# Performance work log

Measured on AMD Instinct MI355X. Metric: run time of the kernel, lower is better.

The kernel has to match this reference:

```python
import jax, jax.numpy as jnp
import numpy as np

TAU = 0.1
HARD_K = 32
MIN_OVERLAP = 4
PAIR_WEIGHTS = [("view", "cart", 0.2), ("cart", "purchase", 1.0), ("view", "purchase", 1.0)]


def setup_inputs() -> dict:
    key = jax.random.key(0)
    ks = jax.random.split(key, 6)
    U, D = 100000, 128
    return {
        "emb_view": jax.random.normal(ks[0], (U, D), dtype=jnp.float32),
        "emb_cart": jax.random.normal(ks[1], (U, D), dtype=jnp.float32),
        "emb_purchase": jax.random.normal(ks[2], (U, D), dtype=jnp.float32),
        "users_view": jax.random.randint(ks[3], (20000,), 0, U, dtype=jnp.int64),
        "users_cart": jax.random.randint(ks[4], (15000,), 0, U, dtype=jnp.int64),
        "users_purchase": jax.random.randint(ks[5], (10000,), 0, U, dtype=jnp.int64),
    }


def _l2norm(x):
    # F.normalize(x, dim=-1): x / max(||x||, eps)
    n = jnp.linalg.norm(x, axis=-1, keepdims=True)
    return x / jnp.maximum(n, 1e-12)


def _directional(z_weak, z_strong, tau, hard_k):
    N = z_strong.shape[0]
    if N < 2:
        return jnp.zeros((), dtype=z_strong.dtype)
    z_w = _l2norm(jax.lax.stop_gradient(z_weak))  # weak side is detached
    z_s = _l2norm(z_strong)
    sim = (z_s @ z_w.T) / tau  # [N, N]
    pos = jnp.diagonal(sim)    # positive logits, labels = arange(N)
    n_hard = min(hard_k, N - 1)
    if 0 < n_hard < N - 1:
        neg_only = jnp.where(jnp.eye(N, dtype=bool), -jnp.inf, sim)
        hard_neg, _ = jax.lax.top_k(neg_only, n_hard)          # [N, n_hard]
        logits = jnp.concatenate([pos[:, None], hard_neg], 1)  # [N, 1+n_hard]
        return jnp.mean(jax.scipy.special.logsumexp(logits, axis=1) - pos)
    # full-softmax CE with label i for row i
    return jnp.mean(jax.scipy.special.logsumexp(sim, axis=1) - pos)


def reference(emb_view, emb_cart, emb_purchase, users_view, users_cart, users_purchase):
    embs = {"view": emb_view, "cart": emb_cart, "purchase": emb_purchase}
    users = {
        "view": np.asarray(users_view),
        "cart": np.asarray(users_cart),
        "purchase": np.asarray(users_purchase),
    }
    loss = jnp.zeros((), dtype=emb_view.dtype)
    for weak, strong, w in PAIR_WEIGHTS:
        u_w, u_s = users[weak], users[strong]
        if u_w.size == 0 or u_s.size == 0:
            continue
        # common_pair = u_w[isin(u_w, u_s)] : keeps u_w order and duplicates
        common = u_w[np.isin(u_w, u_s)]
        if common.size < MIN_OVERLAP:
            continue
        idx = jnp.asarray(common)
        loss = loss + w * _directional(embs[weak][idx], embs[strong][idx], TAU, HARD_K)
    return loss
```

## Files before the change

kernel.cpp:

```cpp
#include <hip/hip_runtime.h>
#include <hip/hip_bf16.h>
#include <math.h>

#define D 128
#define NEG_INF (-3.0e38f)
#define LDA 136
#define MAGIC 0x5CA1AB1Eu

#define C0 3200
#define C1 1792
#define C2 2304
#define T0 25
#define T1 14
#define T2 18
#define NTILES (T0 * T0 + T1 * T1 + T2 * T2)
#define NSEL (C0 / 4 + C1 / 4 + C2 / 4)

typedef __attribute__((ext_vector_type(8))) short bf16x8;
typedef __attribute__((ext_vector_type(8))) unsigned short u16x8;
typedef __attribute__((ext_vector_type(4))) float f32x4;

__device__ __forceinline__ float wredf_add(float v) {
#pragma unroll
  for (int m = 32; m; m >>= 1) v += __shfl_xor(v, m, 64);
  return v;
}
__device__ __forceinline__ float wredf_max(float v) {
#pragma unroll
  for (int m = 32; m; m >>= 1) v = fmaxf(v, __shfl_xor(v, m, 64));
  return v;
}
__device__ __forceinline__ float wredf_min(float v) {
#pragma unroll
  for (int m = 32; m; m >>= 1) v = fminf(v, __shfl_xor(v, m, 64));
  return v;
}
__device__ __forceinline__ int wredi_add(int v) {
#pragma unroll
  for (int m = 32; m; m >>= 1) v += __shfl_xor(v, m, 64);
  return v;
}
__device__ __forceinline__ double wredd_add(double v) {
#pragma unroll
  for (int m = 32; m; m >>= 1) v += __shfl_xor(v, m, 64);
  return v;
}

__global__ void masks_k(const int* __restrict__ uc, int nc,
                        const int* __restrict__ up, int npu,
                        unsigned* __restrict__ mc, unsigned* __restrict__ mp,
                        unsigned long long* __restrict__ header) {
  if (blockIdx.x == 0) header[threadIdx.x] = 0ull;
  int t = blockIdx.x * blockDim.x + threadIdx.x;
  if (t < nc) {
    mc[uc[t]] = MAGIC;
  } else {
    int t2 = t - nc;
    if (t2 < npu) mp[up[t2]] = MAGIC;
  }
}

struct FGArgs {
  const int* src[3];
  int n[3];
  const unsigned* mask[3];
  const float* embW[3];
  const float* embS[3];
  short* zw[3];
  short* zs[3];
  int cap[3];
  int seg1, seg2;
  int* counts;
};

__global__ __launch_bounds__(256) void filtgather_k(FGArgs a) {
  int t = blockIdx.x * 256 + threadIdx.x;
  int lane = threadIdx.x & 63;
  int s, base;
  if (t < a.seg1) { s = 0; base = t; }
  else if (t < a.seg2) { s = 1; base = t - a.seg1; }
  else { s = 2; base = t - a.seg2; }
  bool match = false;
  int u = 0;
  if (base < a.n[s]) {
    u = a.src[s][base];
    match = (a.mask[s][u] == MAGIC);
  }
  unsigned long long b = __ballot(match);
  int tot = __popcll(b);
  if (!tot) return;
  int idx0 = 0;
  if (lane == 0) idx0 = atomicAdd(a.counts + s, tot);
  idx0 = __shfl(idx0, 0, 64);
  const float* eW = a.embW[s];
  const float* eS = a.embS[s];
  short* zw = a.zw[s];
  short* zs = a.zs[s];
  int cap = a.cap[s];
  unsigned long long bb = b;
  for (int k = 0; k < tot; ++k) {
    int sl = __builtin_ctzll(bb);
    bb &= bb - 1;
    int p = idx0 + k;
    if (p >= cap) break;
    int uu = __shfl(u, sl, 64);
    float2 vw = *(const float2*)(eW + (size_t)uu * D + lane * 2);
    float2 vs = *(const float2*)(eS + (size_t)uu * D + lane * 2);
    float ssw = wredf_add(vw.x * vw.x + vw.y * vw.y);
    float sss = wredf_add(vs.x * vs.x + vs.y * vs.y);
    float iw = 1.0f / fmaxf(sqrtf(ssw), 1e-12f);
    float is = 1.0f / fmaxf(sqrtf(sss), 1e-12f);
    __hip_bfloat16 w0 = __float2bfloat16(vw.x * iw), w1 = __float2bfloat16(vw.y * iw);
    __hip_bfloat16 s0 = __float2bfloat16(vs.x * is), s1 = __float2bfloat16(vs.y * is);
    *(ushort2*)(zw + (size_t)p * D + lane * 2) =
        make_ushort2(*(unsigned short*)&w0, *(unsigned short*)&w1);
    *(ushort2*)(zs + (size_t)p * D + lane * 2) =
        make_ushort2(*(unsigned short*)&s0, *(unsigned short*)&s1);
  }
}

struct GemmArgs {
  const short *zs0, *zw0, *zs1, *zw1, *zs2, *zw2;
  unsigned short *s0, *s1, *s2;
  const int* counts;
};

__device__ __forceinline__ void gemm_tile(const short* __restrict__ A, const short* __restrict__ B,
                                          unsigned short* __restrict__ C, int ldc, int bx, int by,
                                          int N, short* As, short* Bs, int tid) {
  int rb = by * 128, cb = bx * 128;
  if (rb >= N || cb >= N) return;
  int rrow = tid >> 4, rcol = (tid & 15) * 8;
#pragma unroll
  for (int pass = 0; pass < 8; ++pass) {
    int row = pass * 16 + rrow;
    uint4 va = *(const uint4*)(A + (size_t)(rb + row) * D + rcol);
    uint4 vb = *(const uint4*)(B + (size_t)(cb + row) * D + rcol);
    *(uint4*)(&As[row * LDA + rcol]) = va;
    *(uint4*)(&Bs[row * LDA + rcol]) = vb;
  }
  __syncthreads();
  int wave = tid >> 6, lane = tid & 63;
  int wr = (wave >> 1) * 64, wc = (wave & 1) * 64;
  int ln = lane & 15, quad = lane >> 4;
  f32x4 acc[4][4] = {};
#pragma unroll
  for (int ks = 0; ks < 4; ++ks) {
    int ko = ks * 32 + quad * 8;
    bf16x8 af[4], bg[4];
#pragma unroll
    for (int i = 0; i < 4; ++i) af[i] = *(const bf16x8*)(&As[(wr + i * 16 + ln) * LDA + ko]);
#pragma unroll
    for (int j = 0; j < 4; ++j) bg[j] = *(const bf16x8*)(&Bs[(wc + j * 16 + ln) * LDA + ko]);
#pragma unroll
    for (int i = 0; i < 4; ++i)
#pragma unroll
      for (int j = 0; j < 4; ++j)
        acc[i][j] = __builtin_amdgcn_mfma_f32_16x16x32_bf16(af[i], bg[j], acc[i][j], 0, 0, 0);
  }
  __syncthreads();
#pragma unroll
  for (int i = 0; i < 4; ++i)
#pragma unroll
    for (int j = 0; j < 4; ++j) {
      int tcol = wc + j * 16 + ln;
#pragma unroll
      for (int r = 0; r < 4; ++r) {
        int trow = wr + i * 16 + quad * 4 + r;
        __hip_bfloat16 h = __float2bfloat16(acc[i][j][r] * 10.0f);
        As[trow * LDA + tcol] = *(short*)&h;
      }
    }
  __syncthreads();
#pragma unroll
  for (int pass = 0; pass < 8; ++pass) {
    int idx = pass * 256 + tid;
    int row = idx >> 4, c8 = (idx & 15) * 8;
    *(uint4*)(C + (size_t)(rb + row) * ldc + cb + c8) = *(const uint4*)(&As[row * LDA + c8]);
  }
  __syncthreads();
}

__global__ __launch_bounds__(256) void gemm_all_k(GemmArgs g) {
  __shared__ __align__(16) short As[128 * LDA];
  __shared__ __align__(16) short Bs[128 * LDA];
  int tid = threadIdx.x;
  int b = blockIdx.x;
  if (b < T0 * T0) {
    int N = min(g.counts[0], C0);
    gemm_tile(g.zs0, g.zw0, g.s0, C0, b % T0, b / T0, N, As, Bs, tid);
  } else if (b < T0 * T0 + T1 * T1) {
    int t = b - T0 * T0;
    int N = min(g.counts[1], C1);
    gemm_tile(g.zs1, g.zw1, g.s1, C1, t % T1, t / T1, N, As, Bs, tid);
  } else {
    int t = b - T0 * T0 - T1 * T1;
    int N = min(g.counts[2], C2);
    gemm_tile(g.zs2, g.zw2, g.s2, C2, t % T2, t / T2, N, As, Bs, tid);
  }
}

template <int NL>
__device__ __forceinline__ void select_rows(const unsigned short* __restrict__ sim, int ldc, int N,
                                            int i, int lane, double* __restrict__ slot) {
  const unsigned short* row = sim + (size_t)i * ldc;
  float vals[NL * 8];
  float posl = NEG_INF;
#pragma unroll
  for (int L = 0; L < NL; ++L) {
    int base = L * 512 + lane * 8;
    u16x8 raw = *(const u16x8*)(row + base);
#pragma unroll
    for (int c = 0; c < 8; ++c) {
      int j = base + c;
      float v = __uint_as_float((unsigned)raw[c] << 16);
      if (L >= NL - 2 && j >= N) v = NEG_INF;
      if (j == i) { posl = v; v = NEG_INF; }
      vals[L * 8 + c] = v;
    }
  }
  float pos = __shfl(posl, (i >> 3) & 63, 64);
  float m = NEG_INF;
#pragma unroll
  for (int s = 0; s < NL * 8; ++s) m = fmaxf(m, vals[s]);
  m = wredf_max(m);
  int K = min(32, N - 1);
  float lo = -10.2f, hi = m + 1e-3f;
  for (int it = 0; it < 12; ++it) {
    float mid = 0.5f * (lo + hi);
    int c = 0;
#pragma unroll
    for (int s = 0; s < NL * 8; ++s) c += (vals[s] > mid) ? 1 : 0;
    c = wredi_add(c);
    if (c >= K) lo = mid; else hi = mid;
  }
  float M = fmaxf(m, pos);
  float sum = 0.0f, vmin = 3.0e38f;
  int cnt = 0;
#pragma unroll
  for (int s = 0; s < NL * 8; ++s) {
    float v = vals[s];
    if (v > lo) {
      sum += __expf(v - M);
      cnt++;
      vmin = fminf(vmin, v);
    }
  }
  sum = wredf_add(sum);
  cnt = wredi_add(cnt);
  vmin = wredf_min(vmin);
  float corr = (cnt > K) ? (float)(cnt - K) * __expf(vmin - M) : 0.0f;
  float lse = M + __logf(sum - corr + __expf(pos - M));
  if (lane == 0) atomicAdd(slot, (double)(lse - pos));
}

__global__ __launch_bounds__(256) void select_k(const unsigned short* __restrict__ sim0,
                                                const unsigned short* __restrict__ sim1,
                                                const unsigned short* __restrict__ sim2,
                                                const int* __restrict__ counts,
                                                double* __restrict__ partials) {
  int wid = threadIdx.x >> 6, lane = threadIdx.x & 63;
  int b = blockIdx.x;
  if (b < C0 / 4) {
    int N = min(counts[0], C0);
    int i = b * 4 + wid;
    if (i < N) {
      double* slot = partials + 0 * 64 + (b & 63);
      if (N <= 3072) select_rows<6>(sim0, C0, N, i, lane, slot);
      else           select_rows<7>(sim0, C0, N, i, lane, slot);
    }
  } else if (b < C0 / 4 + C1 / 4) {
    int bb = b - C0 / 4;
    int N = min(counts[1], C1);
    int i = bb * 4 + wid;
    if (i < N) {
      double* slot = partials + 64 + (bb & 63);
      if (N <= 1536) select_rows<3>(sim1, C1, N, i, lane, slot);
      else           select_rows<4>(sim1, C1, N, i, lane, slot);
    }
  } else {
    int bb = b - C0 / 4 - C1 / 4;
    int N = min(counts[2], C2);
    int i = bb * 4 + wid;
    if (i < N) {
      double* slot = partials + 128 + (bb & 63);
      if (N <= 2048) select_rows<4>(sim2, C2, N, i, lane, slot);
      else           select_rows<5>(sim2, C2, N, i, lane, slot);
    }
  }
}

__global__ void finalize_k(const int* __restrict__ counts, const double* __restrict__ partials,
                           float* __restrict__ out) {
  int wid = threadIdx.x >> 6, lane = threadIdx.x & 63;
  __shared__ double ps[4];
  double v = (threadIdx.x < 192) ? partials[threadIdx.x] : 0.0;
  v = wredd_add(v);
  if (lane == 0 && wid < 3) ps[wid] = v;
  __syncthreads();
  if (threadIdx.x == 0) {
    const float w[3] = {0.2f, 1.0f, 1.0f};
    const int caps[3] = {C0, C1, C2};
    float tot = 0.0f;
    for (int p = 0; p < 3; ++p) {
      int N = min(counts[p], caps[p]);
      if (N >= 4) tot += w[p] * (float)(ps[p] / (double)N);
    }
    out[0] = tot;
  }
}

__global__ void sentinel_k(float* out) {
  if (threadIdx.x == 0 && blockIdx.x == 0) out[0] = -12345.0f;
}

extern "C" void kernel_launch(void* const* d_in, const int* in_sizes, int n_in,
                              void* d_out, int out_size, void* d_ws, size_t ws_size,
                              hipStream_t stream) {
  const float* emb_view = (const float*)d_in[0];
  const float* emb_cart = (const float*)d_in[1];
  const float* emb_pur  = (const float*)d_in[2];
  const int* u_view = (const int*)d_in[3];
  const int* u_cart = (const int*)d_in[4];
  const int* u_pur  = (const int*)d_in[5];
  int nv = in_sizes[3], nc = in_sizes[4], np = in_sizes[5];
  int U = in_sizes[0] / D;

  size_t off = 2048;
  auto alloc = [&](size_t b) {
    size_t o = (off + 255) & ~(size_t)255;
    off = o + b;
    return o;
  };
  size_t mask0_off = alloc((size_t)U * 4);
  size_t mask1_off = alloc((size_t)U * 4);
  size_t zw0_off = alloc((size_t)C0 * D * 2);
  size_t zs0_off = alloc((size_t)C0 * D * 2);
  size_t zw1_off = alloc((size_t)C1 * D * 2);
  size_t zs1_off = alloc((size_t)C1 * D * 2);
  size_t zw2_off = alloc((size_t)C2 * D * 2);
  size_t zs2_off = alloc((size_t)C2 * D * 2);
  size_t sim0_off = alloc((size_t)C0 * C0 * 2);
  size_t sim1_off = alloc((size_t)C1 * C1 * 2);
  size_t sim2_off = alloc((size_t)C2 * C2 * 2);
  (void)alloc(1024);
  int ws_ok = (off <= ws_size) ? 1 : 0;

  char* ws = (char*)d_ws;
  if (!ws_ok) {
    sentinel_k<<<1, 1, 0, stream>>>((float*)d_out);
    return;
  }

  int* counts = (int*)ws;
  double* partials = (double*)(ws + 256);
  unsigned* mask_c = (unsigned*)(ws + mask0_off);
  unsigned* mask_p = (unsigned*)(ws + mask1_off);
  short* zw0 = (short*)(ws + zw0_off);
  short* zs0 = (short*)(ws + zs0_off);
  short* zw1 = (short*)(ws + zw1_off);
  short* zs1 = (short*)(ws + zs1_off);
  short* zw2 = (short*)(ws + zw2_off);
  short* zs2 = (short*)(ws + zs2_off);
  unsigned short* sim0 = (unsigned short*)(ws + sim0_off);
  unsigned short* sim1 = (unsigned short*)(ws + sim1_off);
  unsigned short* sim2 = (unsigned short*)(ws + sim2_off);

  masks_k<<<(nc + np + 255) / 256, 256, 0, stream>>>(u_cart, nc, u_pur, np, mask_c, mask_p,
                                                     (unsigned long long*)ws);

  FGArgs fa;
  fa.src[0] = u_view; fa.n[0] = nv; fa.mask[0] = mask_c;
  fa.embW[0] = emb_view; fa.embS[0] = emb_cart; fa.zw[0] = zw0; fa.zs[0] = zs0; fa.cap[0] = C0;
  fa.src[1] = u_cart; fa.n[1] = nc; fa.mask[1] = mask_p;
  fa.embW[1] = emb_cart; fa.embS[1] = emb_pur; fa.zw[1] = zw1; fa.zs[1] = zs1; fa.cap[1] = C1;
  fa.src[2] = u_view; fa.n[2] = nv; fa.mask[2] = mask_p;
  fa.embW[2] = emb_view; fa.embS[2] = emb_pur; fa.zw[2] = zw2; fa.zs[2] = zs2; fa.cap[2] = C2;
  fa.seg1 = ((nv + 255) / 256) * 256;
  fa.seg2 = fa.seg1 + ((nc + 255) / 256) * 256;
  int t_filt = fa.seg2 + ((nv + 255) / 256) * 256;
  fa.counts = counts;
  filtgather_k<<<t_filt / 256, 256, 0, stream>>>(fa);

  GemmArgs g;
  g.zs0 = zs0; g.zw0 = zw0; g.s0 = sim0;
  g.zs1 = zs1; g.zw1 = zw1; g.s1 = sim1;
  g.zs2 = zs2; g.zw2 = zw2; g.s2 = sim2;
  g.counts = counts;
  gemm_all_k<<<NTILES, 256, 0, stream>>>(g);

  select_k<<<NSEL, 256, 0, stream>>>(sim0, sim1, sim2, counts, partials);

  finalize_k<<<1, 256, 0, stream>>>(counts, partials, (float*)d_out);
}
```

Before: 212.0 us.

## Fuse finalize into persistent select kernel and software-pipeline gather loads

Turns select_k into a grid-stride kernel sized by occupancy, where the last stage is done by block 0 after a spin-wait on a striped completion counter array, removing the separate finalize_k launch. It also double-buffers the embedding row loads in filtgather_k, issuing four gathers ahead of the normalize/convert work to hide load latency. The header zeroing is widened to clear the new counters. The spin-wait assumes every block is co-resident, so the grid size from the occupancy query must hold for correctness, and the extra registers from the load buffers may lower occupancy.

```diff
diff --git a/kernel.cpp b/kernel.cpp
--- a/kernel.cpp
+++ b/kernel.cpp
@@ -50,7 +50,8 @@
                         const int* __restrict__ up, int npu,
                         unsigned* __restrict__ mc, unsigned* __restrict__ mp,
                         unsigned long long* __restrict__ header) {
-  if (blockIdx.x == 0) header[threadIdx.x] = 0ull;
+  if (blockIdx.x == 0)
+    for (int t = threadIdx.x; t < 1024; t += 256) header[t] = 0ull;
   int t = blockIdx.x * blockDim.x + threadIdx.x;
   if (t < nc) {
     mc[uc[t]] = MAGIC;
@@ -97,25 +98,52 @@
   short* zw = a.zw[s];
   short* zs = a.zs[s];
   int cap = a.cap[s];
-  unsigned long long bb = b;
-  for (int k = 0; k < tot; ++k) {
-    int sl = __builtin_ctzll(bb);
-    bb &= bb - 1;
-    int p = idx0 + k;
-    if (p >= cap) break;
-    int uu = __shfl(u, sl, 64);
-    float2 vw = *(const float2*)(eW + (size_t)uu * D + lane * 2);
-    float2 vs = *(const float2*)(eS + (size_t)uu * D + lane * 2);
-    float ssw = wredf_add(vw.x * vw.x + vw.y * vw.y);
-    float sss = wredf_add(vs.x * vs.x + vs.y * vs.y);
-    float iw = 1.0f / fmaxf(sqrtf(ssw), 1e-12f);
-    float is = 1.0f / fmaxf(sqrtf(sss), 1e-12f);
-    __hip_bfloat16 w0 = __float2bfloat16(vw.x * iw), w1 = __float2bfloat16(vw.y * iw);
-    __hip_bfloat16 s0 = __float2bfloat16(vs.x * is), s1 = __float2bfloat16(vs.y * is);
-    *(ushort2*)(zw + (size_t)p * D + lane * 2) =
-        make_ushort2(*(unsigned short*)&w0, *(unsigned short*)&w1);
-    *(ushort2*)(zs + (size_t)p * D + lane * 2) =
-        make_ushort2(*(unsigned short*)&s0, *(unsigned short*)&s1);
+  int kmax = tot;
+  int rem = cap - idx0;
+  if (rem < kmax) kmax = (rem < 0) ? 0 : rem;
+  unsigned long long bbL = b;
+
+  auto ldpair = [&](int k, float2& W, float2& S) {
+    if (k < kmax) {
+      int sl = __builtin_ctzll(bbL);
+      bbL &= bbL - 1;
+      int uu = __shfl(u, sl, 64);
+      W = *(const float2*)(eW + (size_t)uu * D + lane * 2);
+      S = *(const float2*)(eS + (size_t)uu * D + lane * 2);
+    }
+  };
+  auto proc = [&](int k, float2 vw, float2 vs) {
+    if (k < kmax) {
+      int p = idx0 + k;
+      float ssw = wredf_add(vw.x * vw.x + vw.y * vw.y);
+      float sss = wredf_add(vs.x * vs.x + vs.y * vs.y);
+      float iw = 1.0f / fmaxf(sqrtf(ssw), 1e-12f);
+      float is = 1.0f / fmaxf(sqrtf(sss), 1e-12f);
+      __hip_bfloat16 w0 = __float2bfloat16(vw.x * iw), w1 = __float2bfloat16(vw.y * iw);
+      __hip_bfloat16 s0 = __float2bfloat16(vs.x * is), s1 = __float2bfloat16(vs.y * is);
+      *(ushort2*)(zw + (size_t)p * D + lane * 2) =
+          make_ushort2(*(unsigned short*)&w0, *(unsigned short*)&w1);
+      *(ushort2*)(zs + (size_t)p * D + lane * 2) =
+          make_ushort2(*(unsigned short*)&s0, *(unsigned short*)&s1);
+    }
+  };
+
+  float2 Aw0 = {}, Aw1 = {}, Aw2 = {}, Aw3 = {}, Asv0 = {}, Asv1 = {}, Asv2 = {}, Asv3 = {};
+  float2 Bw0 = {}, Bw1 = {}, Bw2 = {}, Bw3 = {}, Bsv0 = {}, Bsv1 = {}, Bsv2 = {}, Bsv3 = {};
+  int kb = 0;
+  ldpair(0, Aw0, Asv0); ldpair(1, Aw1, Asv1); ldpair(2, Aw2, Asv2); ldpair(3, Aw3, Asv3);
+  while (kb < kmax) {
+    ldpair(kb + 4, Bw0, Bsv0); ldpair(kb + 5, Bw1, Bsv1);
+    ldpair(kb + 6, Bw2, Bsv2); ldpair(kb + 7, Bw3, Bsv3);
+    proc(kb + 0, Aw0, Asv0); proc(kb + 1, Aw1, Asv1);
+    proc(kb + 2, Aw2, Asv2); proc(kb + 3, Aw3, Asv3);
+    kb += 4;
+    if (kb >= kmax) break;
+    ldpair(kb + 4, Aw0, Asv0); ldpair(kb + 5, Aw1, Asv1);
+    ldpair(kb + 6, Aw2, Asv2); ldpair(kb + 7, Aw3, Asv3);
+    proc(kb + 0, Bw0, Bsv0); proc(kb + 1, Bw1, Bsv1);
+    proc(kb + 2, Bw2, Bsv2); proc(kb + 3, Bw3, Bsv3);
+    kb += 4;
   }
 }
 
@@ -254,13 +282,12 @@
   if (lane == 0) atomicAdd(slot, (double)(lse - pos));
 }
 
-__global__ __launch_bounds__(256) void select_k(const unsigned short* __restrict__ sim0,
-                                                const unsigned short* __restrict__ sim1,
-                                                const unsigned short* __restrict__ sim2,
-                                                const int* __restrict__ counts,
-                                                double* __restrict__ partials) {
-  int wid = threadIdx.x >> 6, lane = threadIdx.x & 63;
-  int b = blockIdx.x;
+__device__ __forceinline__ void select_body(int b, int wid, int lane,
+                                            const unsigned short* __restrict__ sim0,
+                                            const unsigned short* __restrict__ sim1,
+                                            const unsigned short* __restrict__ sim2,
+                                            const int* __restrict__ counts,
+                                            double* __restrict__ partials) {
   if (b < C0 / 4) {
     int N = min(counts[0], C0);
     int i = b * 4 + wid;
@@ -290,23 +317,52 @@
   }
 }
 
-__global__ void finalize_k(const int* __restrict__ counts, const double* __restrict__ partials,
-                           float* __restrict__ out) {
-  int wid = threadIdx.x >> 6, lane = threadIdx.x & 63;
-  __shared__ double ps[4];
-  double v = (threadIdx.x < 192) ? partials[threadIdx.x] : 0.0;
-  v = wredd_add(v);
-  if (lane == 0 && wid < 3) ps[wid] = v;
+__global__ __launch_bounds__(256) void select_k(const unsigned short* __restrict__ sim0,
+                                                const unsigned short* __restrict__ sim1,
+                                                const unsigned short* __restrict__ sim2,
+                                                const int* __restrict__ counts,
+                                                double* __restrict__ partials,
+                                                int* __restrict__ cntC,
+                                                float* __restrict__ out) {
+  int tid = threadIdx.x, wid = tid >> 6, lane = tid & 63;
+  int nb = gridDim.x;
+  for (int b = blockIdx.x; b < NSEL; b += nb)
+    select_body(b, wid, lane, sim0, sim1, sim2, counts, partials);
   __syncthreads();
-  if (threadIdx.x == 0) {
-    const float w[3] = {0.2f, 1.0f, 1.0f};
-    const int caps[3] = {C0, C1, C2};
-    float tot = 0.0f;
-    for (int p = 0; p < 3; ++p) {
-      int N = min(counts[p], caps[p]);
-      if (N >= 4) tot += w[p] * (float)(ps[p] / (double)N);
-    }
-    out[0] = tot;
+  if (tid == 0) {
+    __builtin_amdgcn_fence(__ATOMIC_RELEASE, "agent");
+    __hip_atomic_fetch_add(&cntC[(blockIdx.x & 63) * 16], 1, __ATOMIC_RELAXED,
+                           __HIP_MEMORY_SCOPE_AGENT);
+  }
+  if (blockIdx.x == 0) {
+    if (tid < 64) {
+      for (;;) {
+        int s = __hip_atomic_load(&cntC[tid * 16], __ATOMIC_RELAXED, __HIP_MEMORY_SCOPE_AGENT);
+        s = wredi_add(s);
+        if (s >= nb) break;
+        __builtin_amdgcn_s_sleep(2);
+      }
+    }
+    __syncthreads();
+    if (tid == 0) __builtin_amdgcn_fence(__ATOMIC_ACQUIRE, "agent");
+    __syncthreads();
+    __shared__ double ps[4];
+    double v = (tid < 192)
+                   ? __hip_atomic_load(&partials[tid], __ATOMIC_RELAXED, __HIP_MEMORY_SCOPE_AGENT)
+                   : 0.0;
+    v = wredd_add(v);
+    if (lane == 0 && wid < 3) ps[wid] = v;
+    __syncthreads();
+    if (tid == 0) {
+      const float w[3] = {0.2f, 1.0f, 1.0f};
+      const int caps[3] = {C0, C1, C2};
+      float tot = 0.0f;
+      for (int p = 0; p < 3; ++p) {
+        int N = min(counts[p], caps[p]);
+        if (N >= 4) tot += w[p] * (float)(ps[p] / (double)N);
+      }
+      out[0] = tot;
+    }
   }
 }
 
@@ -326,7 +382,7 @@
   int nv = in_sizes[3], nc = in_sizes[4], np = in_sizes[5];
   int U = in_sizes[0] / D;
 
-  size_t off = 2048;
+  size_t off = 8192;
   auto alloc = [&](size_t b) {
     size_t o = (off + 255) & ~(size_t)255;
     off = o + b;
@@ -353,7 +409,8 @@
   }
 
   int* counts = (int*)ws;
-  double* partials = (double*)(ws + 256);
+  int* cntC = (int*)(ws + 1024);
+  double* partials = (double*)(ws + 5632);
   unsigned* mask_c = (unsigned*)(ws + mask0_off);
   unsigned* mask_p = (unsigned*)(ws + mask1_off);
   short* zw0 = (short*)(ws + zw0_off);
@@ -389,7 +446,14 @@
   g.counts = counts;
   gemm_all_k<<<NTILES, 256, 0, stream>>>(g);
 
-  select_k<<<NSEL, 256, 0, stream>>>(sim0, sim1, sim2, counts, partials);
-
-  finalize_k<<<1, 256, 0, stream>>>(counts, partials, (float*)d_out);
-}
+  static int s_gC = 0;
+  if (s_gC == 0) {
+    int nb = 0;
+    if (hipOccupancyMaxActiveBlocksPerMultiprocessor(
+            &nb, reinterpret_cast<const void*>(select_k), 256, 0) != hipSuccess || nb < 1)
+      nb = 1;
+    long gsz = (long)nb * 256;
+    s_gC = (int)((gsz < NSEL) ? gsz : NSEL);
+  }
+  select_k<<<s_gC, 256, 0, stream>>>(sim0, sim1, sim2, counts, partials, cntC, (float*)d_out);
+}
```

New measurement: 232.9 us. 1.1x slower.
